# Optimization experiments

Measured on AMD Instinct MI355X. Metric: run time of the kernel, lower is better.

Reference implementation:

```python
import jax, jax.numpy as jnp
import numpy as np

N, K, H = 98, 10, 4        # landmarks, neighbors/node, heads
B, CIN, HC = 1024, 256, 64 # batch, in_channels, head_channels
NEG = -9e15


def setup_inputs() -> dict:
    key = jax.random.key(0)
    ks = jax.random.split(key, 3)
    rng = np.random.default_rng(0)
    # fixed sparsity pattern: K unique neighbors per row, row-major order
    cols2d = np.stack([np.sort(rng.choice(N, K, replace=False)) for _ in range(N)])
    rows = np.repeat(np.arange(N), K)
    cols = cols2d.reshape(-1)
    x = jax.random.normal(ks[0], (B, N, CIN), jnp.float32)
    W = jax.random.normal(ks[1], (H, 2, CIN, HC), jnp.float32) * 0.05  # xavier-ish
    e = jnp.ones((H, N * K), jnp.float32)  # nn.init.constant_(e, 1)
    stdv = 1.0 / np.sqrt(HC)
    bias = jax.random.uniform(ks[2], (H, HC), jnp.float32, -stdv, stdv)
    return {"x": x, "W": W, "e": e, "bias": bias,
            "rows": jnp.asarray(rows, jnp.int32),
            "cols": jnp.asarray(cols, jnp.int32)}


def reference(x, W, e, bias, rows, cols):
    # h0/h1 for all heads at once: [2, H, B, N, HC]
    h = jnp.einsum('bnc,hscd->shbnd', x, W)
    h0, h1 = h[0], h[1]
    # masked adjacency logits per head: -9e15 everywhere, learned e at edges
    base = jnp.full((N, N), NEG, jnp.float32)
    logits = jax.vmap(lambda eh: base.at[rows, cols].set(eh))(e)  # [H,N,N]
    A = jax.nn.softmax(logits, axis=-1)  # F.softmax(adj, dim=1) on [N,N]
    diag = jnp.diagonal(A, axis1=-2, axis2=-1)  # [H,N] -> adj*M part
    A_off = A - diag[..., None] * jnp.eye(N, dtype=A.dtype)  # adj*(1-M)
    out = diag[:, None, :, None] * h0 + jnp.einsum('hij,hbjd->hbid', A_off, h1)
    out = out + bias[:, None, None, :]  # [H,B,N,HC]
    # concat heads along channel dim -> [B, N, H*HC]
    return jnp.transpose(out, (1, 2, 0, 3)).reshape(B, N, H * HC)
```

## Files before the change

### kernel.cpp

```cpp
#include <hip/hip_runtime.h>

typedef __bf16 bf16;
typedef bf16 bf16x4 __attribute__((ext_vector_type(4)));
typedef bf16 bf16x8 __attribute__((ext_vector_type(8)));
typedef float f32x4 __attribute__((ext_vector_type(4)));

#define NND 98
#define KNB 10
#define NH 4
#define CIN 256
#define HC 64
#define XROW_B 528
#define CROW_E 136

__global__ __launch_bounds__(256) void prep_wp_kernel(const float* __restrict__ W,
                                                      bf16* __restrict__ Wp) {
  int t = blockIdx.x * 256 + threadIdx.x;
  if (t >= 8 * 8 * 4 * 64) return;
  int lane = t & 63;
  int nt = (t >> 6) & 3;
  int kt = (t >> 8) & 7;
  int hs = t >> 11;
  int n = nt * 16 + (lane & 15);
  int kb = kt * 32 + (lane >> 4) * 8;
  const float* src = W + (hs * CIN + kb) * HC + n;
  bf16x8 v;
#pragma unroll
  for (int j = 0; j < 8; ++j) v[j] = (bf16)src[j * HC];
  *(bf16x8*)(Wp + (long long)t * 8) = v;
}

__global__ __launch_bounds__(1024, 4) void semgconv_kernel(
    const float* __restrict__ x, const float* __restrict__ e,
    const float* __restrict__ bias, const int* __restrict__ cols,
    const bf16* __restrict__ Wp, float* __restrict__ out) {
  __shared__ __align__(16) unsigned char reg0[112 * XROW_B];
  __shared__ float w_lds[NND * KNB];
  __shared__ short cols_lds[NND * KNB];
  __shared__ float diag_lds[NND];

  const int tid = threadIdx.x;
  const int b = blockIdx.x;

  if (tid < NND) {
    const int* cp = cols + tid * KNB;
#pragma unroll
    for (int j = 0; j < KNB; ++j) cols_lds[tid * KNB + j] = (short)cp[j];
  }

  {
    const float* xb = x + (long long)b * NND * CIN;
#pragma unroll
    for (int it = 0; it < 7; ++it) {
      int idx = tid + it * 1024;
      int n = idx >> 6;
      int c4 = (idx & 63) << 2;
      f32x4 v = {0.f, 0.f, 0.f, 0.f};
      if (n < NND) v = *(const f32x4*)(xb + n * CIN + c4);
      bf16x4 bv;
      bv[0] = (bf16)v[0]; bv[1] = (bf16)v[1]; bv[2] = (bf16)v[2]; bv[3] = (bf16)v[3];
      *(bf16x4*)(reg0 + n * XROW_B + c4 * 2) = bv;
    }
  }
  __syncthreads();

  const int lane = tid & 63;
  const int wv = tid >> 6;
  const int wh = wv & 3;
  const int wm = wv >> 2;
  const int mt0 = wm * 2;

  f32x4 acc[2][8] = {};
  const unsigned char* aptr = reg0 + (mt0 * 16 + (lane & 15)) * XROW_B + (lane >> 4) * 16;
  const bf16* wpl = Wp + ((long long)(wh * 2) * (8 * 4 * 64) + lane) * 8;

#pragma unroll
  for (int kt = 0; kt < 8; ++kt) {
    bf16x8 afr[2];
#pragma unroll
    for (int im = 0; im < 2; ++im)
      if (mt0 + im < 7)
        afr[im] = *(const bf16x8*)(aptr + im * (16 * XROW_B) + kt * 64);
    {
      bf16x8 bfr[4];
#pragma unroll
      for (int nt = 0; nt < 4; ++nt)
        bfr[nt] = *(const bf16x8*)(wpl + ((kt * 4 + nt) * 64) * 8);
#pragma unroll
      for (int im = 0; im < 2; ++im)
        if (mt0 + im < 7)
#pragma unroll
          for (int nt = 0; nt < 4; ++nt)
            acc[im][nt] = __builtin_amdgcn_mfma_f32_16x16x32_bf16(afr[im], bfr[nt],
                                                                  acc[im][nt], 0, 0, 0);
    }
    {
      bf16x8 bfr[4];
#pragma unroll
      for (int nt = 0; nt < 4; ++nt)
        bfr[nt] = *(const bf16x8*)(wpl + ((8 * 4 + kt * 4 + nt) * 64) * 8);
#pragma unroll
      for (int im = 0; im < 2; ++im)
        if (mt0 + im < 7)
#pragma unroll
          for (int nt = 0; nt < 4; ++nt)
            acc[im][4 + nt] = __builtin_amdgcn_mfma_f32_16x16x32_bf16(afr[im], bfr[nt],
                                                                      acc[im][4 + nt], 0, 0, 0);
    }
  }
  __syncthreads();

  bf16* C = (bf16*)reg0;
  const int ig = tid >> 4;
  const int d4 = (tid & 15) * 4;

  for (int h = 0; h < NH; ++h) {
    if (tid < NND) {
      const int i = tid;
      const float* ep = e + (h * NND + i) * KNB;
      float ev[KNB];
      float mx = -3.0e38f;
#pragma unroll
      for (int j = 0; j < KNB; ++j) { ev[j] = ep[j]; mx = fmaxf(mx, ev[j]); }
      float s = 0.f;
#pragma unroll
      for (int j = 0; j < KNB; ++j) { ev[j] = __expf(ev[j] - mx); s += ev[j]; }
      const float inv = 1.f / s;
      float dg = 0.f;
#pragma unroll
      for (int j = 0; j < KNB; ++j) {
        float wvv = ev[j] * inv;
        if ((int)cols_lds[i * KNB + j] == i) { dg = wvv; wvv = 0.f; }
        w_lds[i * KNB + j] = wvv;
      }
      diag_lds[i] = dg;
    }
    if (wh == h) {
#pragma unroll
      for (int im = 0; im < 2; ++im) {
        int mt = mt0 + im;
        if (mt < 7) {
          int rowb = mt * 16 + (lane >> 4) * 4;
#pragma unroll
          for (int q = 0; q < 8; ++q) {
            int col = q * 16 + (lane & 15);
#pragma unroll
            for (int r = 0; r < 4; ++r)
              C[(rowb + r) * CROW_E + col] = (bf16)acc[im][q][r];
          }
        }
      }
    }
    __syncthreads();

    {
      f32x4 bs = *(const f32x4*)(bias + h * HC + d4);
      float* outp = out + (long long)b * NND * (NH * HC) + h * HC + d4;
#pragma unroll
      for (int ib = 0; ib < 2; ++ib) {
        int i = ib * 64 + ig;
        if (i < NND) {
          f32x4 av = bs;
          float dg = diag_lds[i];
          bf16x4 c0 = *(const bf16x4*)(C + i * CROW_E + d4);
          av[0] += dg * (float)c0[0];
          av[1] += dg * (float)c0[1];
          av[2] += dg * (float)c0[2];
          av[3] += dg * (float)c0[3];
#pragma unroll
          for (int j = 0; j < KNB; ++j) {
            float wj = w_lds[i * KNB + j];
            int cj = (int)cols_lds[i * KNB + j];
            bf16x4 c1 = *(const bf16x4*)(C + cj * CROW_E + HC + d4);
            av[0] += wj * (float)c1[0];
            av[1] += wj * (float)c1[1];
            av[2] += wj * (float)c1[2];
            av[3] += wj * (float)c1[3];
          }
          *(f32x4*)(outp + (long long)i * (NH * HC)) = av;
        }
      }
    }
    __syncthreads();
  }
}

extern "C" void kernel_launch(void* const* d_in, const int* in_sizes, int n_in,
                              void* d_out, int out_size, void* d_ws, size_t ws_size,
                              hipStream_t stream) {
  const float* x    = (const float*)d_in[0];
  const float* W    = (const float*)d_in[1];
  const float* e    = (const float*)d_in[2];
  const float* bias = (const float*)d_in[3];
  const int* cols   = (const int*)d_in[5];
  float* out        = (float*)d_out;
  bf16* Wp          = (bf16*)d_ws;

  int B = in_sizes[0] / (NND * CIN);

  prep_wp_kernel<<<64, 256, 0, stream>>>(W, Wp);
  semgconv_kernel<<<B, 1024, 0, stream>>>(x, e, bias, cols, Wp, out);
}
```

Baseline: 257.8 us.

## Replace sparse neighbor aggregation with dense MFMA over precomputed adjacency matrix

Builds a dense per-head bf16 matrix [diag | off-diagonal weights] (98x224 padded) in prep kernels, prepacked in MFMA fragment layout. The main kernel then computes the aggregation as a second MFMA GEMM over the transposed h0/h1 tile, so the per-block softmax and the scalar gather loop over neighbors go away. Two heads are processed per round instead of one, which halves the barrier rounds. In exchange it does many more FLOPs on mostly-zero data, writes output with scattered scalar stores instead of float4, and adds three tiny launches.

```diff
diff --git a/kernel.cpp b/kernel.cpp
--- a/kernel.cpp
+++ b/kernel.cpp
@@ -11,7 +11,12 @@
 #define CIN 256
 #define HC 64
 #define XROW_B 528
-#define CROW_E 136
+#define C1TS 232
+#define M2K 224
+#define M2ROWS 112
+
+#define WS_M2D_OFF 262144
+#define WS_M2P_OFF 462848
 
 __global__ __launch_bounds__(256) void prep_wp_kernel(const float* __restrict__ W,
                                                       bf16* __restrict__ Wp) {
@@ -30,23 +35,67 @@
   *(bf16x8*)(Wp + (long long)t * 8) = v;
 }
 
+__global__ __launch_bounds__(256) void prep_zero_kernel(unsigned int* __restrict__ M2d_u32) {
+  int t = blockIdx.x * 256 + threadIdx.x;
+  if (t < NH * M2ROWS * M2K / 2) M2d_u32[t] = 0u;
+}
+
+__global__ __launch_bounds__(256) void prep_scatter_kernel(const float* __restrict__ e,
+                                                           const int* __restrict__ cols,
+                                                           bf16* __restrict__ M2d) {
+  int t = blockIdx.x * 256 + threadIdx.x;
+  if (t >= NH * NND) return;
+  int h = t / NND, i = t % NND;
+  const float* ep = e + (h * NND + i) * KNB;
+  const int* cp = cols + i * KNB;
+  float ev[KNB]; int cv[KNB];
+  float mx = -3.0e38f;
+#pragma unroll
+  for (int j = 0; j < KNB; ++j) { ev[j] = ep[j]; cv[j] = cp[j]; mx = fmaxf(mx, ev[j]); }
+  float s = 0.f;
+#pragma unroll
+  for (int j = 0; j < KNB; ++j) { ev[j] = __expf(ev[j] - mx); s += ev[j]; }
+  const float inv = 1.f / s;
+  bf16* row = M2d + ((long long)h * M2ROWS + i) * M2K;
+  float dg = 0.f;
+#pragma unroll
+  for (int j = 0; j < KNB; ++j) {
+    float wv = ev[j] * inv;
+    if (cv[j] == i) { dg = wv; }
+    else            { row[112 + cv[j]] = (bf16)wv; }
+  }
+  row[i] = (bf16)dg;
+}
+
+__global__ __launch_bounds__(256) void prep_m2p_kernel(const bf16* __restrict__ M2d,
+                                                       bf16* __restrict__ M2p) {
+  int t = blockIdx.x * 256 + threadIdx.x;
+  if (t >= NH * 7 * 7 * 64) return;
+  int lane = t & 63;
+  int u = t >> 6;
+  int kt = u % 7; u /= 7;
+  int mt = u % 7;
+  int h = u / 7;
+  int m = mt * 16 + (lane & 15);
+  int kb = kt * 32 + (lane >> 4) * 8;
+  const bf16* src = M2d + ((long long)h * M2ROWS + m) * M2K + kb;
+  bf16x8 v = *(const bf16x8*)src;
+  *(bf16x8*)(M2p + (long long)t * 8) = v;
+}
+
 __global__ __launch_bounds__(1024, 4) void semgconv_kernel(
-    const float* __restrict__ x, const float* __restrict__ e,
-    const float* __restrict__ bias, const int* __restrict__ cols,
-    const bf16* __restrict__ Wp, float* __restrict__ out) {
-  __shared__ __align__(16) unsigned char reg0[112 * XROW_B];
-  __shared__ float w_lds[NND * KNB];
-  __shared__ short cols_lds[NND * KNB];
-  __shared__ float diag_lds[NND];
+    const float* __restrict__ x, const float* __restrict__ bias,
+    const bf16* __restrict__ Wp, const bf16* __restrict__ M2p,
+    float* __restrict__ out) {
+  __shared__ __align__(16) unsigned char reg0[2 * 64 * C1TS * 2];
 
   const int tid = threadIdx.x;
   const int b = blockIdx.x;
-
-  if (tid < NND) {
-    const int* cp = cols + tid * KNB;
-#pragma unroll
-    for (int j = 0; j < KNB; ++j) cols_lds[tid * KNB + j] = (short)cp[j];
-  }
+  const int lane = tid & 63;
+  const int wv = tid >> 6;
+  const int wh = wv & 3;
+  const int wm = wv >> 2;
+  const int mt0 = wm * 2;
 
   {
     const float* xb = x + (long long)b * NND * CIN;
@@ -64,12 +113,6 @@
   }
   __syncthreads();
 
-  const int lane = tid & 63;
-  const int wv = tid >> 6;
-  const int wh = wv & 3;
-  const int wm = wv >> 2;
-  const int mt0 = wm * 2;
-
   f32x4 acc[2][8] = {};
   const unsigned char* aptr = reg0 + (mt0 * 16 + (lane & 15)) * XROW_B + (lane >> 4) * 16;
   const bf16* wpl = Wp + ((long long)(wh * 2) * (8 * 4 * 64) + lane) * 8;
@@ -110,75 +153,55 @@
   }
   __syncthreads();
 
-  bf16* C = (bf16*)reg0;
-  const int ig = tid >> 4;
-  const int d4 = (tid & 15) * 4;
-
-  for (int h = 0; h < NH; ++h) {
-    if (tid < NND) {
-      const int i = tid;
-      const float* ep = e + (h * NND + i) * KNB;
-      float ev[KNB];
-      float mx = -3.0e38f;
-#pragma unroll
-      for (int j = 0; j < KNB; ++j) { ev[j] = ep[j]; mx = fmaxf(mx, ev[j]); }
-      float s = 0.f;
-#pragma unroll
-      for (int j = 0; j < KNB; ++j) { ev[j] = __expf(ev[j] - mx); s += ev[j]; }
-      const float inv = 1.f / s;
-      float dg = 0.f;
-#pragma unroll
-      for (int j = 0; j < KNB; ++j) {
-        float wvv = ev[j] * inv;
-        if ((int)cols_lds[i * KNB + j] == i) { dg = wvv; wvv = 0.f; }
-        w_lds[i * KNB + j] = wvv;
-      }
-      diag_lds[i] = dg;
-    }
-    if (wh == h) {
+  bf16* C1T = (bf16*)reg0;
+
+  for (int r = 0; r < 2; ++r) {
+    if ((wh >> 1) == r) {
+      bf16* ct = C1T + (wh & 1) * (64 * C1TS);
 #pragma unroll
       for (int im = 0; im < 2; ++im) {
         int mt = mt0 + im;
         if (mt < 7) {
-          int rowb = mt * 16 + (lane >> 4) * 4;
+          int kb = mt * 16 + ((lane >> 4) * 4);
 #pragma unroll
           for (int q = 0; q < 8; ++q) {
-            int col = q * 16 + (lane & 15);
-#pragma unroll
-            for (int r = 0; r < 4; ++r)
-              C[(rowb + r) * CROW_E + col] = (bf16)acc[im][q][r];
+            int ch = (q & 3) * 16 + (lane & 15);
+            int kk = (q >> 2) * 112 + kb;
+            bf16x4 v;
+            v[0] = (bf16)acc[im][q][0];
+            v[1] = (bf16)acc[im][q][1];
+            v[2] = (bf16)acc[im][q][2];
+            v[3] = (bf16)acc[im][q][3];
+            *(bf16x4*)(ct + ch * C1TS + kk) = v;
           }
         }
       }
     }
     __syncthreads();
 
-    {
-      f32x4 bs = *(const f32x4*)(bias + h * HC + d4);
-      float* outp = out + (long long)b * NND * (NH * HC) + h * HC + d4;
-#pragma unroll
-      for (int ib = 0; ib < 2; ++ib) {
-        int i = ib * 64 + ig;
-        if (i < NND) {
-          f32x4 av = bs;
-          float dg = diag_lds[i];
-          bf16x4 c0 = *(const bf16x4*)(C + i * CROW_E + d4);
-          av[0] += dg * (float)c0[0];
-          av[1] += dg * (float)c0[1];
-          av[2] += dg * (float)c0[2];
-          av[3] += dg * (float)c0[3];
-#pragma unroll
-          for (int j = 0; j < KNB; ++j) {
-            float wj = w_lds[i * KNB + j];
-            int cj = (int)cols_lds[i * KNB + j];
-            bf16x4 c1 = *(const bf16x4*)(C + cj * CROW_E + HC + d4);
-            av[0] += wj * (float)c1[0];
-            av[1] += wj * (float)c1[1];
-            av[2] += wj * (float)c1[2];
-            av[3] += wj * (float)c1[3];
-          }
-          *(f32x4*)(outp + (long long)i * (NH * HC)) = av;
-        }
+    for (int t = wv; t < 56; t += 16) {
+      int hl = t / 28;
+      int rem = t % 28;
+      int mt = rem >> 2, nt = rem & 3;
+      int h = r * 2 + hl;
+      const bf16* ct = C1T + hl * (64 * C1TS)
+                     + (nt * 16 + (lane & 15)) * C1TS + ((lane >> 4) * 8);
+      const bf16* ap = M2p + (((long long)(h * 7 + mt) * 7) * 64 + lane) * 8;
+      f32x4 a2 = {0.f, 0.f, 0.f, 0.f};
+#pragma unroll
+      for (int kt = 0; kt < 7; ++kt) {
+        bf16x8 af = *(const bf16x8*)(ap + (long long)kt * (64 * 8));
+        bf16x8 bfv = *(const bf16x8*)(ct + kt * 32);
+        a2 = __builtin_amdgcn_mfma_f32_16x16x32_bf16(af, bfv, a2, 0, 0, 0);
+      }
+      int colg = h * HC + nt * 16 + (lane & 15);
+      float bs = bias[colg];
+      int rowb = mt * 16 + (lane >> 4) * 4;
+      float* op = out + (long long)b * (NND * NH * HC) + colg;
+#pragma unroll
+      for (int r4 = 0; r4 < 4; ++r4) {
+        int node = rowb + r4;
+        if (node < NND) op[(long long)node * (NH * HC)] = a2[r4] + bs;
       }
     }
     __syncthreads();
@@ -194,10 +217,16 @@
   const float* bias = (const float*)d_in[3];
   const int* cols   = (const int*)d_in[5];
   float* out        = (float*)d_out;
-  bf16* Wp          = (bf16*)d_ws;
+
+  bf16* Wp  = (bf16*)d_ws;
+  bf16* M2d = (bf16*)((char*)d_ws + WS_M2D_OFF);
+  bf16* M2p = (bf16*)((char*)d_ws + WS_M2P_OFF);
 
   int B = in_sizes[0] / (NND * CIN);
 
   prep_wp_kernel<<<64, 256, 0, stream>>>(W, Wp);
-  semgconv_kernel<<<B, 1024, 0, stream>>>(x, e, bias, cols, Wp, out);
-}
+  prep_zero_kernel<<<(NH * M2ROWS * M2K / 2 + 255) / 256, 256, 0, stream>>>((unsigned int*)M2d);
+  prep_scatter_kernel<<<2, 256, 0, stream>>>(e, cols, M2d);
+  prep_m2p_kernel<<<(NH * 7 * 7 * 64 + 255) / 256, 256, 0, stream>>>(M2d, M2p);
+  semgconv_kernel<<<B, 1024, 0, stream>>>(x, bias, Wp, M2p, out);
+}
```

After: 264.7 us. +2.6%, slower.
